# Optimization experiments

Hardware: AMD Instinct MI355X
Metric: run time of the kernel (lower is better)

## Reference

```python
import jax, jax.numpy as jnp
import numpy as np

BLOCK_SPLIT = (4, 4, 4)
GRID = 256
N_BLOCK = 64
BX = GRID // 4  # 64, per-block grid resolution along each axis
N_PTS = 4_194_304


def setup_inputs() -> dict:
    key = jax.random.key(0)
    k1, k2 = jax.random.split(key)
    aabb = jnp.array([[-1.5, -1.5, -1.5], [1.5, 1.5, 1.5]], dtype=jnp.float32)
    # points roughly inside the aabb
    xyz_sampled = jax.random.uniform(k1, (N_PTS, 3), dtype=jnp.float32) * 3.0 - 1.5
    alpha_volume = jax.random.uniform(k2, (GRID, GRID, GRID), dtype=jnp.float32)
    # per-block domains (as kilonerf global_to_local expects): block AABBs
    idx = np.stack(np.meshgrid(np.arange(4), np.arange(4), np.arange(4), indexing='ij'), -1).reshape(-1, 3)
    voxel = np.array([3.0 / 4.0] * 3)
    dmin = (-1.5 + idx * voxel).astype(np.float32)
    dmax = (dmin + voxel).astype(np.float32)
    return {"xyz_sampled": xyz_sampled, "aabb": aabb, "alpha_volume": alpha_volume,
            "domain_min": jnp.asarray(dmin), "domain_max": jnp.asarray(dmax)}


def _sample_alpha(xyz, aabb, alpha_volume, dmin, dmax):
    bs = jnp.asarray(BLOCK_SPLIT, jnp.float32)
    voxel = (aabb[1] - aabb[0]) / bs                      # per-block world size
    idx3 = jnp.floor((xyz - aabb[0]) / voxel).astype(jnp.int32)
    idx3 = jnp.clip(idx3, 0, jnp.array(BLOCK_SPLIT, jnp.int32) - 1)  # edge clamp (matches loop)
    strides = jnp.array([BLOCK_SPLIT[2] * BLOCK_SPLIT[1], BLOCK_SPLIT[2], 1], jnp.int32)
    bid = (idx3 * strides).sum(-1)                        # [N] block id in [0, 64)

    order = jnp.argsort(bid)                              # jax sort is stable; matches bucket-by-block order
    bid_s = bid[order]
    pts = xyz[order]

    # global_to_local (kilonerf): map into per-block [-1,1]^3
    local = 2.0 * (pts - dmin[bid_s]) / (dmax[bid_s] - dmin[bid_s]) - 1.0  # [N,3] (gx,gy,gz)

    # torch .view(64,1,64,64,64) is a raw contiguous reinterpretation -> plain reshape
    vols = alpha_volume.reshape(N_BLOCK, BX, BX, BX)      # [B, D, H, W]
    D = H = W = BX
    # grid_sample convention: grid x -> W axis, y -> H axis, z -> D axis; align_corners=True
    fx = (local[:, 0] + 1.0) * 0.5 * (W - 1)
    fy = (local[:, 1] + 1.0) * 0.5 * (H - 1)
    fz = (local[:, 2] + 1.0) * 0.5 * (D - 1)
    x0 = jnp.floor(fx); y0 = jnp.floor(fy); z0 = jnp.floor(fz)
    wx = fx - x0; wy = fy - y0; wz = fz - z0
    x0i = x0.astype(jnp.int32); y0i = y0.astype(jnp.int32); z0i = z0.astype(jnp.int32)

    def fetch(zi, yi, xi):
        # zeros padding for out-of-range corners (grid_sample padding_mode='zeros')
        inb = (zi >= 0) & (zi < D) & (yi >= 0) & (yi < H) & (xi >= 0) & (xi < W)
        v = vols[bid_s, jnp.clip(zi, 0, D - 1), jnp.clip(yi, 0, H - 1), jnp.clip(xi, 0, W - 1)]
        return jnp.where(inb, v, 0.0)

    out = jnp.zeros_like(fx)
    for dz, wz_ in ((0, 1.0 - wz), (1, wz)):
        for dy, wy_ in ((0, 1.0 - wy), (1, wy)):
            for dx, wx_ in ((0, 1.0 - wx), (1, wx)):
                out = out + wz_ * wy_ * wx_ * fetch(z0i + dz, y0i + dy, x0i + dx)
    return out  # [N] alpha values in block-sorted order


def reference(xyz_sampled, aabb, alpha_volume, domain_min, domain_max):
    return _sample_alpha(xyz_sampled, aabb, alpha_volume, domain_min, domain_max)
```

## Files before the change

kernel.cpp:

```cpp
#include <hip/hip_runtime.h>

#define NB     64
#define NF     4096
#define TILE   16384
#define HBLK   1024
#define DBLK   1024
#define FBLK   512
#define GBLK   256
#define SBLK   256
#define FB_TILE 4096
#define STAGE_HALF 8192

#define GLOBAL_AS __attribute__((address_space(1)))
#define LDS_AS    __attribute__((address_space(3)))

__device__ __forceinline__ int compute_bid(float px, float py, float pz,
                                           float a0x, float a0y, float a0z,
                                           float vx, float vy, float vz) {
    int ix = (int)floorf((px - a0x) / vx);
    int iy = (int)floorf((py - a0y) / vy);
    int iz = (int)floorf((pz - a0z) / vz);
    ix = min(max(ix, 0), 3);
    iy = min(max(iy, 0), 3);
    iz = min(max(iz, 0), 3);
    return ix * 16 + iy * 4 + iz;
}

__device__ __forceinline__ void quant_point(float px, float py, float pz,
        float a0x, float a0y, float a0z, float vx, float vy, float vz,
        const float* s_dn, const float* s_sc,
        int& b, int& qx, int& qy, int& qz, int& key) {
    b = compute_bid(px, py, pz, a0x, a0y, a0z, vx, vy, vz);
    float fx = (px - s_dn[3 * b])     * s_sc[3 * b];
    float fy = (py - s_dn[3 * b + 1]) * s_sc[3 * b + 1];
    float fz = (pz - s_dn[3 * b + 2]) * s_sc[3 * b + 2];
    qx = min(max(__float2int_rn(fx * 256.0f), 0), 16128);
    qy = min(max(__float2int_rn(fy * 256.0f), 0), 16128);
    qz = min(max(__float2int_rn(fz * 256.0f), 0), 16128);
    key = (b << 6) | ((qz >> 12) << 4) | ((qy >> 12) << 2) | (qx >> 12);
}

__global__ void __launch_bounds__(HBLK) hist_kernel(
        const float* __restrict__ xyz, const float* __restrict__ aabb,
        const float* __restrict__ dmin, const float* __restrict__ dmax,
        int* __restrict__ hist64, int* __restrict__ tot4096, int N, int T) {
    __shared__ int   sh[NF];
    __shared__ float s_dn[192], s_sc[192];
    const int tid = threadIdx.x, g = blockIdx.x;
    for (int l = tid; l < NF; l += HBLK) sh[l] = 0;
    if (tid < 192) { s_dn[tid] = dmin[tid]; s_sc[tid] = 63.0f / (dmax[tid] - dmin[tid]); }
    const float a0x = aabb[0], a0y = aabb[1], a0z = aabb[2];
    const float vx = (aabb[3] - a0x) * 0.25f;
    const float vy = (aabb[4] - a0y) * 0.25f;
    const float vz = (aabb[5] - a0z) * 0.25f;
    __syncthreads();
    for (int c = 0; c < TILE / (HBLK * 4); ++c) {
        int p0 = g * TILE + c * (HBLK * 4) + tid * 4;
        int b, qx, qy, qz, k;
        if (p0 + 3 < N) {
            const float4* v4 = (const float4*)(xyz + (size_t)p0 * 3);
            float4 f0 = v4[0], f1 = v4[1], f2 = v4[2];
            quant_point(f0.x, f0.y, f0.z, a0x, a0y, a0z, vx, vy, vz, s_dn, s_sc, b, qx, qy, qz, k);
            atomicAdd(&sh[k], 1);
            quant_point(f0.w, f1.x, f1.y, a0x, a0y, a0z, vx, vy, vz, s_dn, s_sc, b, qx, qy, qz, k);
            atomicAdd(&sh[k], 1);
            quant_point(f1.z, f1.w, f2.x, a0x, a0y, a0z, vx, vy, vz, s_dn, s_sc, b, qx, qy, qz, k);
            atomicAdd(&sh[k], 1);
            quant_point(f2.y, f2.z, f2.w, a0x, a0y, a0z, vx, vy, vz, s_dn, s_sc, b, qx, qy, qz, k);
            atomicAdd(&sh[k], 1);
        } else {
            for (int t = 0; t < 4; ++t) {
                int i = p0 + t;
                if (i < N) {
                    quant_point(xyz[3 * i], xyz[3 * i + 1], xyz[3 * i + 2],
                                a0x, a0y, a0z, vx, vy, vz, s_dn, s_sc, b, qx, qy, qz, k);
                    atomicAdd(&sh[k], 1);
                }
            }
        }
    }
    __syncthreads();
    for (int l = tid; l < NF; l += HBLK) {
        int c = sh[l];
        if (c) atomicAdd(&tot4096[l], c);
    }
    if (tid < NB) {
        int s = 0;
        #pragma unroll
        for (int j = 0; j < 64; ++j) s += sh[tid * 64 + j];
        hist64[tid * T + g] = s;
    }
}

__global__ void scans_kernel(int* __restrict__ hist64, int* __restrict__ tot64,
                             const int* __restrict__ tot4096,
                             int* __restrict__ foff, int* __restrict__ fcnt, int G) {
    __shared__ int sh[SBLK];
    const int t = threadIdx.x;
    if (blockIdx.x < NB) {
        const int b = blockIdx.x;
        const int L = (G + SBLK - 1) / SBLK;
        const int lo = t * L;
        const int n = min(L, max(0, G - lo));
        const int base = b * G + lo;
        int s = 0;
        for (int k = 0; k < n; ++k) s += hist64[base + k];
        sh[t] = s;
        __syncthreads();
        for (int off = 1; off < SBLK; off <<= 1) {
            int v = (t >= off) ? sh[t - off] : 0;
            __syncthreads();
            sh[t] += v;
            __syncthreads();
        }
        int excl = (t == 0) ? 0 : sh[t - 1];
        for (int k = 0; k < n; ++k) {
            int v = hist64[base + k];
            hist64[base + k] = excl;
            excl += v;
        }
        if (t == SBLK - 1) tot64[b] = sh[SBLK - 1];
    } else {
        const int L = NF / SBLK;
        int loc[16];
        int s = 0;
        #pragma unroll
        for (int j = 0; j < L; ++j) { loc[j] = tot4096[t * L + j]; s += loc[j]; }
        sh[t] = s;
        __syncthreads();
        for (int o = 1; o < SBLK; o <<= 1) {
            int v = (t >= o) ? sh[t - o] : 0;
            __syncthreads();
            sh[t] += v;
            __syncthreads();
        }
        int run = (t == 0) ? 0 : sh[t - 1];
        #pragma unroll
        for (int j = 0; j < L; ++j) {
            foff[t * L + j] = run;
            fcnt[t * L + j] = run;
            run += loc[j];
        }
        if (t == SBLK - 1) foff[NF] = run;
    }
}

__global__ void __launch_bounds__(DBLK) scatterC_kernel(
        const float* __restrict__ xyz, const float* __restrict__ aabb,
        const float* __restrict__ dmin, const float* __restrict__ dmax,
        const int* __restrict__ hist64, const int* __restrict__ tot64,
        unsigned long long* __restrict__ payloadC, int N, int T) {
    __shared__ unsigned long long stage[STAGE_HALF];
    __shared__ int   s_wh[16][NB];
    __shared__ int   s_cnt0[NB];
    __shared__ int   s_off[NB];
    __shared__ int   s_start[NB];
    __shared__ int   s_gb[NB];
    __shared__ float s_dn[192], s_sc[192];
    const int tid = threadIdx.x, g = blockIdx.x;
    const int lane = tid & 63, wv = tid >> 6;
    if (tid < NB) s_off[tid] = tot64[tid];
    if (tid < 192) { s_dn[tid] = dmin[tid]; s_sc[tid] = 63.0f / (dmax[tid] - dmin[tid]); }
    ((int*)s_wh)[tid] = 0;
    const float a0x = aabb[0], a0y = aabb[1], a0z = aabb[2];
    const float vx = (aabb[3] - a0x) * 0.25f;
    const float vy = (aabb[4] - a0y) * 0.25f;
    const float vz = (aabb[5] - a0z) * 0.25f;
    __syncthreads();
    for (int o = 1; o < NB; o <<= 1) {
        int v = (tid < NB && tid >= o) ? s_off[tid - o] : 0;
        __syncthreads();
        if (tid < NB) s_off[tid] += v;
        __syncthreads();
    }
    if (tid < NB) s_cnt0[tid] = hist64[tid * T + g] + (tid ? s_off[tid - 1] : 0);

    const unsigned long long lt = (1ull << lane) - 1ull;
    const int base_i = g * TILE + wv * 1024;
    unsigned long long cache[16];
    #pragma unroll
    for (int r = 0; r < 16; ++r) {
        int i = base_i + r * 64 + lane;
        bool valid = (i < N);
        int b = 0, qx = 0, qy = 0, qz = 0, key;
        if (valid) {
            quant_point(xyz[3 * i], xyz[3 * i + 1], xyz[3 * i + 2],
                        a0x, a0y, a0z, vx, vy, vz, s_dn, s_sc, b, qx, qy, qz, key);
        }
        unsigned long long m = __ballot(valid);
        #pragma unroll
        for (int q = 0; q < 6; ++q) {
            unsigned long long bal = __ballot((b >> q) & 1);
            m &= ((b >> q) & 1) ? bal : ~bal;
        }
        int rank = __popcll(m & lt);
        int run = valid ? s_wh[wv][b] : 0;
        if (valid && rank == 0) s_wh[wv][b] = run + __popcll(m);
        int localpos = run + rank;
        cache[r] = (unsigned long long)(unsigned)qx
                 | ((unsigned long long)(unsigned)qy << 14)
                 | ((unsigned long long)(unsigned)qz << 28)
                 | ((unsigned long long)(unsigned)b  << 42)
                 | ((unsigned long long)(unsigned)localpos << 48);
    }
    __syncthreads();
    for (int o = 1; o < 16; o <<= 1) {
        int v = (wv >= o) ? s_wh[wv - o][lane] : 0;
        __syncthreads();
        s_wh[wv][lane] += v;
        __syncthreads();
    }
    if (wv == 0) {
        int v = s_wh[15][lane];
        int incl = v;
        #pragma unroll
        for (int o = 1; o < 64; o <<= 1) {
            int u = __shfl_up(incl, o);
            if (lane >= o) incl += u;
        }
        int excl = incl - v;
        s_start[lane] = excl;
        s_gb[lane] = s_cnt0[lane] - excl;
    }
    __syncthreads();
    const int n = min(TILE, N - g * TILE);
    #pragma unroll
    for (int r = 0; r < 16; ++r) {
        int i = base_i + r * 64 + lane;
        if (i < N) {
            unsigned long long cc = cache[r];
            int b = (int)((cc >> 42) & 63);
            int localpos = (int)((cc >> 48) & 1023);
            int lidx = s_start[b] + (wv ? s_wh[wv - 1][b] : 0) + localpos;
            unsigned long long p48 = cc & ((1ull << 48) - 1);
            if (lidx < STAGE_HALF) stage[lidx] = p48;
            cache[r] = p48 | ((unsigned long long)(unsigned)lidx << 48);
        }
    }
    __syncthreads();
    {
        int nA = min(n, STAGE_HALF);
        for (int j = tid; j < nA; j += DBLK) {
            unsigned long long p = stage[j];
            int b = (int)((p >> 42) & 63);
            payloadC[s_gb[b] + j] = p;
        }
    }
    __syncthreads();
    #pragma unroll
    for (int r = 0; r < 16; ++r) {
        int i = base_i + r * 64 + lane;
        if (i < N) {
            unsigned long long cc = cache[r];
            int lidx = (int)(cc >> 48);
            if (lidx >= STAGE_HALF)
                stage[lidx - STAGE_HALF] = cc & ((1ull << 48) - 1);
        }
    }
    __syncthreads();
    for (int j = STAGE_HALF + tid; j < n; j += DBLK) {
        unsigned long long p = stage[j - STAGE_HALF];
        int b = (int)((p >> 42) & 63);
        payloadC[s_gb[b] + j] = p;
    }
}

__global__ void __launch_bounds__(FBLK) scatterF_kernel(
        const unsigned long long* __restrict__ payloadC,
        int* __restrict__ fcnt,
        unsigned long long* __restrict__ payloadF, int N) {
    __shared__ int s_fb[NF];
    const int tid = threadIdx.x, t2 = blockIdx.x;
    for (int l = tid; l < NF; l += FBLK) s_fb[l] = 0;
    __syncthreads();
    const int lo = t2 * TILE;
    const int n = min(TILE, N - lo);
    for (int j0 = tid * 4; j0 < n; j0 += FBLK * 4) {
        unsigned long long p[4];
        int m;
        if (j0 + 3 < n) {
            m = 4;
            ulonglong2 a = *(const ulonglong2*)(payloadC + lo + j0);
            ulonglong2 b2 = *(const ulonglong2*)(payloadC + lo + j0 + 2);
            p[0] = a.x; p[1] = a.y; p[2] = b2.x; p[3] = b2.y;
        } else {
            m = n - j0;
            for (int t = 0; t < m; ++t) p[t] = payloadC[lo + j0 + t];
        }
        for (int t = 0; t < m; ++t) {
            unsigned long long pp = p[t];
            int qx = (int)(pp & 16383), qy = (int)((pp >> 14) & 16383);
            int qz = (int)((pp >> 28) & 16383), b = (int)((pp >> 42) & 63);
            int key = (b << 6) | ((qz >> 12) << 4) | ((qy >> 12) << 2) | (qx >> 12);
            atomicAdd(&s_fb[key], 1);
        }
    }
    __syncthreads();
    for (int l = tid; l < NF; l += FBLK) {
        int c = s_fb[l];
        s_fb[l] = c ? atomicAdd(&fcnt[l], c) : 0;
    }
    __syncthreads();
    for (int j0 = tid * 4; j0 < n; j0 += FBLK * 4) {
        unsigned long long p[4];
        int m;
        if (j0 + 3 < n) {
            m = 4;
            ulonglong2 a = *(const ulonglong2*)(payloadC + lo + j0);
            ulonglong2 b2 = *(const ulonglong2*)(payloadC + lo + j0 + 2);
            p[0] = a.x; p[1] = a.y; p[2] = b2.x; p[3] = b2.y;
        } else {
            m = n - j0;
            for (int t = 0; t < m; ++t) p[t] = payloadC[lo + j0 + t];
        }
        for (int t = 0; t < m; ++t) {
            unsigned long long pp = p[t];
            int qx = (int)(pp & 16383), qy = (int)((pp >> 14) & 16383);
            int qz = (int)((pp >> 28) & 16383), b = (int)((pp >> 42) & 63);
            int key = (b << 6) | ((qz >> 12) << 4) | ((qy >> 12) << 2) | (qx >> 12);
            int fpos = atomicAdd(&s_fb[key], 1);
            payloadF[fpos] = (pp & ((1ull << 42) - 1))
                           | ((unsigned long long)(unsigned)(lo + j0 + t) << 42);
        }
    }
}

__global__ void __launch_bounds__(GBLK) gather_kernel(
        const float* __restrict__ vol,
        const unsigned long long* __restrict__ payloadF,
        const int* __restrict__ foff, const float* __restrict__ zf,
        float* __restrict__ out) {
    __shared__ float sv[77 * 64];
    const int tid = threadIdx.x;
    const int lane = tid & 63, wv = tid >> 6;
    const int nb = gridDim.x, d = blockIdx.x;
    const int k = (nb % 8 == 0) ? (d % 8) * (nb / 8) + (d / 8) : d;
    const int b = k >> 6;
    const int bz = ((k >> 4) & 3) * 16, by = ((k >> 2) & 3) * 16, bx = (k & 3) * 16;
    const float* vb = vol + ((size_t)b << 18);
    for (int m = wv; m < 77; m += GBLK / 64) {
        int l = m * 64 + lane;
        int z = l / 289, r = l - z * 289, y = r / 17, x = r - y * 17;
        int gz = bz + z, gy = by + y, gx = bx + x;
        bool ok = (l < 17 * 17 * 17) && (gz < 64) && (gy < 64) && (gx < 64);
        const float* src = ok ? (vb + ((gz << 12) + (gy << 6) + gx)) : zf;
        __builtin_amdgcn_global_load_lds((const GLOBAL_AS void*)src,
                                         (LDS_AS void*)(sv + m * 64), 4, 0, 0);
    }
    __syncthreads();
    const int lo = foff[k];
    const int n = foff[k + 1] - lo;
    for (int j0 = tid * 4; j0 < n; j0 += GBLK * 4) {
        unsigned long long p[4];
        int m;
        if (j0 + 3 < n) {
            m = 4;
            ulonglong2 a = *(const ulonglong2*)(payloadF + lo + j0);
            ulonglong2 b2 = *(const ulonglong2*)(payloadF + lo + j0 + 2);
            p[0] = a.x; p[1] = a.y; p[2] = b2.x; p[3] = b2.y;
        } else {
            m = n - j0;
            for (int t = 0; t < m; ++t) p[t] = payloadF[lo + j0 + t];
        }
        #pragma unroll 4
        for (int t = 0; t < m; ++t) {
            unsigned long long pp = p[t];
            int qx = (int)(pp & 16383), qy = (int)((pp >> 14) & 16383);
            int qz = (int)((pp >> 28) & 16383);
            int pos = (int)(pp >> 42);
            float wx = (qx & 255) * (1.0f / 256.0f);
            float wy = (qy & 255) * (1.0f / 256.0f);
            float wz = (qz & 255) * (1.0f / 256.0f);
            int lx = (qx >> 8) - bx, ly = (qy >> 8) - by, lz = (qz >> 8) - bz;
            int base = lz * 289 + ly * 17 + lx;
            float v000 = sv[base],       v001 = sv[base + 1];
            float v010 = sv[base + 17],  v011 = sv[base + 18];
            float v100 = sv[base + 289], v101 = sv[base + 290];
            float v110 = sv[base + 306], v111 = sv[base + 307];
            float c00 = v000 + wx * (v001 - v000);
            float c01 = v010 + wx * (v011 - v010);
            float c10 = v100 + wx * (v101 - v100);
            float c11 = v110 + wx * (v111 - v110);
            float c0 = c00 + wy * (c01 - c00);
            float c1 = c10 + wy * (c11 - c10);
            out[pos] = c0 + wz * (c1 - c0);
        }
    }
}

__global__ void fb_hist_kernel(const float* __restrict__ xyz,
                               const float* __restrict__ aabb,
                               int* __restrict__ hist, int N, int G) {
    __shared__ int s_h[NB];
    const int tid = threadIdx.x, g = blockIdx.x;
    if (tid < NB) s_h[tid] = 0;
    __syncthreads();
    const float a0x = aabb[0], a0y = aabb[1], a0z = aabb[2];
    const float vx = (aabb[3] - a0x) * 0.25f;
    const float vy = (aabb[4] - a0y) * 0.25f;
    const float vz = (aabb[5] - a0z) * 0.25f;
    for (int c = 0; c < FB_TILE / 256; ++c) {
        int i = g * FB_TILE + c * 256 + tid;
        if (i < N)
            atomicAdd(&s_h[compute_bid(xyz[3 * i], xyz[3 * i + 1], xyz[3 * i + 2],
                                       a0x, a0y, a0z, vx, vy, vz)], 1);
    }
    __syncthreads();
    if (tid < NB) hist[tid * G + g] = s_h[tid];
}

__global__ void fb_scan_kernel(int* __restrict__ hist, int* __restrict__ tot, int G) {
    __shared__ int sh[SBLK];
    const int b = blockIdx.x, t = threadIdx.x;
    const int L = (G + SBLK - 1) / SBLK;
    const int lo = t * L;
    const int n = min(L, max(0, G - lo));
    const int base = b * G + lo;
    int s = 0;
    for (int k = 0; k < n; ++k) s += hist[base + k];
    sh[t] = s;
    __syncthreads();
    for (int off = 1; off < SBLK; off <<= 1) {
        int v = (t >= off) ? sh[t - off] : 0;
        __syncthreads();
        sh[t] += v;
        __syncthreads();
    }
    int excl = (t == 0) ? 0 : sh[t - 1];
    for (int k = 0; k < n; ++k) {
        int v = hist[base + k];
        hist[base + k] = excl;
        excl += v;
    }
    if (t == SBLK - 1) tot[b] = sh[SBLK - 1];
}

__global__ void fb_scatter_kernel(const float* __restrict__ xyz,
                                  const float* __restrict__ aabb,
                                  const float* __restrict__ dmin,
                                  const float* __restrict__ dmax,
                                  const float* __restrict__ vol,
                                  const int* __restrict__ hist,
                                  const int* __restrict__ tot64,
                                  float* __restrict__ out, int N, int G) {
    __shared__ int   s_cnt[NB], s_off[NB];
    __shared__ int   s_whist[4][NB];
    __shared__ float s_dn[192], s_sc[192];
    const int tid = threadIdx.x, g = blockIdx.x;
    if (tid < NB) s_off[tid] = tot64[tid];
    if (tid < 192) { s_dn[tid] = dmin[tid]; s_sc[tid] = 63.0f / (dmax[tid] - dmin[tid]); }
    __syncthreads();
    for (int o = 1; o < NB; o <<= 1) {
        int v = (tid < NB && tid >= o) ? s_off[tid - o] : 0;
        __syncthreads();
        if (tid < NB) s_off[tid] += v;
        __syncthreads();
    }
    if (tid < NB) s_cnt[tid] = hist[tid * G + g] + (tid ? s_off[tid - 1] : 0);
    const float a0x = aabb[0], a0y = aabb[1], a0z = aabb[2];
    const float vx = (aabb[3] - a0x) * 0.25f;
    const float vy = (aabb[4] - a0y) * 0.25f;
    const float vz = (aabb[5] - a0z) * 0.25f;
    __syncthreads();
    const int lane = tid & 63, wv = tid >> 6;
    const unsigned long long lt = (1ull << lane) - 1ull;
    for (int c = 0; c < FB_TILE / 256; ++c) {
        int i = g * FB_TILE + c * 256 + tid;
        bool valid = (i < N);
        int b = 0;
        float alpha = 0.0f;
        if (valid) {
            float px = xyz[3 * i], py = xyz[3 * i + 1], pz = xyz[3 * i + 2];
            b = compute_bid(px, py, pz, a0x, a0y, a0z, vx, vy, vz);
            float fx = (px - s_dn[3 * b])     * s_sc[3 * b];
            float fy = (py - s_dn[3 * b + 1]) * s_sc[3 * b + 1];
            float fz = (pz - s_dn[3 * b + 2]) * s_sc[3 * b + 2];
            float x0f = floorf(fx), y0f = floorf(fy), z0f = floorf(fz);
            float wx = fx - x0f, wy = fy - y0f, wz = fz - z0f;
            int x0 = (int)x0f, y0 = (int)y0f, z0 = (int)z0f;
            const float* vb = vol + ((size_t)b << 18);
            auto F = [&](int zi, int yi, int xi) -> float {
                if ((unsigned)zi >= 64u || (unsigned)yi >= 64u || (unsigned)xi >= 64u)
                    return 0.0f;
                return vb[(zi << 12) + (yi << 6) + xi];
            };
            float s = 0.0f;
            s += (1.0f - wz) * (1.0f - wy) * (1.0f - wx) * F(z0,     y0,     x0);
            s += (1.0f - wz) * (1.0f - wy) * wx          * F(z0,     y0,     x0 + 1);
            s += (1.0f - wz) * wy          * (1.0f - wx) * F(z0,     y0 + 1, x0);
            s += (1.0f - wz) * wy          * wx          * F(z0,     y0 + 1, x0 + 1);
            s += wz          * (1.0f - wy) * (1.0f - wx) * F(z0 + 1, y0,     x0);
            s += wz          * (1.0f - wy) * wx          * F(z0 + 1, y0,     x0 + 1);
            s += wz          * wy          * (1.0f - wx) * F(z0 + 1, y0 + 1, x0);
            s += wz          * wy          * wx          * F(z0 + 1, y0 + 1, x0 + 1);
            alpha = s;
        }
        ((int*)s_whist)[tid] = 0;
        __syncthreads();
        unsigned long long m = __ballot(valid);
        #pragma unroll
        for (int q = 0; q < 6; ++q) {
            unsigned long long bal = __ballot((b >> q) & 1);
            m &= ((b >> q) & 1) ? bal : ~bal;
        }
        int rank = __popcll(m & lt);
        if (valid && rank == 0) s_whist[wv][b] = __popcll(m);
        __syncthreads();
        if (valid) {
            int pos = s_cnt[b] + rank;
            for (int w2 = 0; w2 < wv; ++w2) pos += s_whist[w2][b];
            out[pos] = alpha;
        }
        __syncthreads();
        if (tid < NB)
            s_cnt[tid] += s_whist[0][tid] + s_whist[1][tid] +
                          s_whist[2][tid] + s_whist[3][tid];
        __syncthreads();
    }
}

extern "C" void kernel_launch(void* const* d_in, const int* in_sizes, int n_in,
                              void* d_out, int out_size, void* d_ws, size_t ws_size,
                              hipStream_t stream) {
    const float* xyz  = (const float*)d_in[0];
    const float* aabb = (const float*)d_in[1];
    const float* vol  = (const float*)d_in[2];
    const float* dmin = (const float*)d_in[3];
    const float* dmax = (const float*)d_in[4];
    float* out = (float*)d_out;
    const int N = in_sizes[0] / 3;
    const int T = (N + TILE - 1) / TILE;

    auto align = [](size_t x) { return (x + 255) & ~(size_t)255; };
    char* ws = (char*)d_ws;
    size_t o = 0;
    unsigned long long* payloadC = (unsigned long long*)(ws + o); o += align((size_t)N * 8);
    unsigned long long* payloadF = (unsigned long long*)(ws + o); o += align((size_t)N * 8);
    int* hist64  = (int*)(ws + o); o += align((size_t)NB * T * 4);
    int* tot64   = (int*)(ws + o); o += 256;
    size_t zbase = o;
    int* tot4096 = (int*)(ws + o); o += align((size_t)NF * 4);
    int* foff    = (int*)(ws + o); o += align((size_t)(NF + 1) * 4);
    int* fcnt    = (int*)(ws + o); o += align((size_t)NF * 4);
    float* zf    = (float*)(ws + o); o += 256;
    size_t zlen = o - zbase;
    const bool fine = (N <= (1 << 22)) && (ws_size >= o);

    if (fine) {
        hipMemsetAsync(ws + zbase, 0, zlen, stream);
        hist_kernel<<<T, HBLK, 0, stream>>>(xyz, aabb, dmin, dmax,
                                            hist64, tot4096, N, T);
        scans_kernel<<<NB + 1, SBLK, 0, stream>>>(hist64, tot64, tot4096,
                                                  foff, fcnt, T);
        scatterC_kernel<<<T, DBLK, 0, stream>>>(xyz, aabb, dmin, dmax,
                                                hist64, tot64, payloadC, N, T);
        scatterF_kernel<<<T, FBLK, 0, stream>>>(payloadC, fcnt, payloadF, N);
        gather_kernel<<<NF, GBLK, 0, stream>>>(vol, payloadF, foff, zf, out);
    } else {
        const int Gf = (N + FB_TILE - 1) / FB_TILE;
        int* h = (int*)ws;
        int* t = (int*)(ws + align((size_t)NB * Gf * 4));
        fb_hist_kernel<<<Gf, 256, 0, stream>>>(xyz, aabb, h, N, Gf);
        fb_scan_kernel<<<NB, SBLK, 0, stream>>>(h, t, Gf);
        fb_scatter_kernel<<<Gf, 256, 0, stream>>>(xyz, aabb, dmin, dmax, vol,
                                                  h, t, out, N, Gf);
    }
}
```

Measured before the change: 252.8 us.

## Fuse histogram, scans and coarse scatter into one cooperative grid-synced kernel

Replaces the separate hist, scans and scatterC launches with a single cooperative kernel that keeps each tile's points quantized in registers, builds both histograms, uses grid.sync to run the prefix scans in the first 65 blocks, and then scatters. This removes one full read of xyz, one recomputation of the quantization and two kernel launches. scatterF now uses 1024 threads and keeps its payload in registers instead of re-reading it for the second pass. Risks include the cost of grid-wide barriers, whether all 256 blocks of 1024 threads with larger LDS can be co-resident, and higher register pressure.

```diff
diff --git a/kernel.cpp b/kernel.cpp
--- a/kernel.cpp
+++ b/kernel.cpp
@@ -1,11 +1,11 @@
 #include <hip/hip_runtime.h>
+#include <hip/hip_cooperative_groups.h>
 
 #define NB     64
 #define NF     4096
 #define TILE   16384
-#define HBLK   1024
 #define DBLK   1024
-#define FBLK   512
+#define FBLK   1024
 #define GBLK   256
 #define SBLK   256
 #define FB_TILE 4096
@@ -13,6 +13,8 @@
 
 #define GLOBAL_AS __attribute__((address_space(1)))
 #define LDS_AS    __attribute__((address_space(3)))
+
+namespace cg = cooperative_groups;
 
 __device__ __forceinline__ int compute_bid(float px, float py, float pz,
                                            float a0x, float a0y, float a0z,
@@ -40,117 +42,16 @@
     key = (b << 6) | ((qz >> 12) << 4) | ((qy >> 12) << 2) | (qx >> 12);
 }
 
-__global__ void __launch_bounds__(HBLK) hist_kernel(
+__global__ void __launch_bounds__(DBLK) coop_kernel(
         const float* __restrict__ xyz, const float* __restrict__ aabb,
         const float* __restrict__ dmin, const float* __restrict__ dmax,
-        int* __restrict__ hist64, int* __restrict__ tot4096, int N, int T) {
-    __shared__ int   sh[NF];
-    __shared__ float s_dn[192], s_sc[192];
-    const int tid = threadIdx.x, g = blockIdx.x;
-    for (int l = tid; l < NF; l += HBLK) sh[l] = 0;
-    if (tid < 192) { s_dn[tid] = dmin[tid]; s_sc[tid] = 63.0f / (dmax[tid] - dmin[tid]); }
-    const float a0x = aabb[0], a0y = aabb[1], a0z = aabb[2];
-    const float vx = (aabb[3] - a0x) * 0.25f;
-    const float vy = (aabb[4] - a0y) * 0.25f;
-    const float vz = (aabb[5] - a0z) * 0.25f;
-    __syncthreads();
-    for (int c = 0; c < TILE / (HBLK * 4); ++c) {
-        int p0 = g * TILE + c * (HBLK * 4) + tid * 4;
-        int b, qx, qy, qz, k;
-        if (p0 + 3 < N) {
-            const float4* v4 = (const float4*)(xyz + (size_t)p0 * 3);
-            float4 f0 = v4[0], f1 = v4[1], f2 = v4[2];
-            quant_point(f0.x, f0.y, f0.z, a0x, a0y, a0z, vx, vy, vz, s_dn, s_sc, b, qx, qy, qz, k);
-            atomicAdd(&sh[k], 1);
-            quant_point(f0.w, f1.x, f1.y, a0x, a0y, a0z, vx, vy, vz, s_dn, s_sc, b, qx, qy, qz, k);
-            atomicAdd(&sh[k], 1);
-            quant_point(f1.z, f1.w, f2.x, a0x, a0y, a0z, vx, vy, vz, s_dn, s_sc, b, qx, qy, qz, k);
-            atomicAdd(&sh[k], 1);
-            quant_point(f2.y, f2.z, f2.w, a0x, a0y, a0z, vx, vy, vz, s_dn, s_sc, b, qx, qy, qz, k);
-            atomicAdd(&sh[k], 1);
-        } else {
-            for (int t = 0; t < 4; ++t) {
-                int i = p0 + t;
-                if (i < N) {
-                    quant_point(xyz[3 * i], xyz[3 * i + 1], xyz[3 * i + 2],
-                                a0x, a0y, a0z, vx, vy, vz, s_dn, s_sc, b, qx, qy, qz, k);
-                    atomicAdd(&sh[k], 1);
-                }
-            }
-        }
-    }
-    __syncthreads();
-    for (int l = tid; l < NF; l += HBLK) {
-        int c = sh[l];
-        if (c) atomicAdd(&tot4096[l], c);
-    }
-    if (tid < NB) {
-        int s = 0;
-        #pragma unroll
-        for (int j = 0; j < 64; ++j) s += sh[tid * 64 + j];
-        hist64[tid * T + g] = s;
-    }
-}
-
-__global__ void scans_kernel(int* __restrict__ hist64, int* __restrict__ tot64,
-                             const int* __restrict__ tot4096,
-                             int* __restrict__ foff, int* __restrict__ fcnt, int G) {
-    __shared__ int sh[SBLK];
-    const int t = threadIdx.x;
-    if (blockIdx.x < NB) {
-        const int b = blockIdx.x;
-        const int L = (G + SBLK - 1) / SBLK;
-        const int lo = t * L;
-        const int n = min(L, max(0, G - lo));
-        const int base = b * G + lo;
-        int s = 0;
-        for (int k = 0; k < n; ++k) s += hist64[base + k];
-        sh[t] = s;
-        __syncthreads();
-        for (int off = 1; off < SBLK; off <<= 1) {
-            int v = (t >= off) ? sh[t - off] : 0;
-            __syncthreads();
-            sh[t] += v;
-            __syncthreads();
-        }
-        int excl = (t == 0) ? 0 : sh[t - 1];
-        for (int k = 0; k < n; ++k) {
-            int v = hist64[base + k];
-            hist64[base + k] = excl;
-            excl += v;
-        }
-        if (t == SBLK - 1) tot64[b] = sh[SBLK - 1];
-    } else {
-        const int L = NF / SBLK;
-        int loc[16];
-        int s = 0;
-        #pragma unroll
-        for (int j = 0; j < L; ++j) { loc[j] = tot4096[t * L + j]; s += loc[j]; }
-        sh[t] = s;
-        __syncthreads();
-        for (int o = 1; o < SBLK; o <<= 1) {
-            int v = (t >= o) ? sh[t - o] : 0;
-            __syncthreads();
-            sh[t] += v;
-            __syncthreads();
-        }
-        int run = (t == 0) ? 0 : sh[t - 1];
-        #pragma unroll
-        for (int j = 0; j < L; ++j) {
-            foff[t * L + j] = run;
-            fcnt[t * L + j] = run;
-            run += loc[j];
-        }
-        if (t == SBLK - 1) foff[NF] = run;
-    }
-}
-
-__global__ void __launch_bounds__(DBLK) scatterC_kernel(
-        const float* __restrict__ xyz, const float* __restrict__ aabb,
-        const float* __restrict__ dmin, const float* __restrict__ dmax,
-        const int* __restrict__ hist64, const int* __restrict__ tot64,
+        int* __restrict__ hist64, int* __restrict__ tot64,
+        int* __restrict__ tot4096, int* __restrict__ foff,
+        int* __restrict__ fcnt,
         unsigned long long* __restrict__ payloadC, int N, int T) {
+    cg::grid_group grid = cg::this_grid();
     __shared__ unsigned long long stage[STAGE_HALF];
+    __shared__ int   s_fb[NF];
     __shared__ int   s_wh[16][NB];
     __shared__ int   s_cnt0[NB];
     __shared__ int   s_off[NB];
@@ -159,21 +60,14 @@
     __shared__ float s_dn[192], s_sc[192];
     const int tid = threadIdx.x, g = blockIdx.x;
     const int lane = tid & 63, wv = tid >> 6;
-    if (tid < NB) s_off[tid] = tot64[tid];
     if (tid < 192) { s_dn[tid] = dmin[tid]; s_sc[tid] = 63.0f / (dmax[tid] - dmin[tid]); }
     ((int*)s_wh)[tid] = 0;
+    for (int l = tid; l < NF; l += DBLK) s_fb[l] = 0;
     const float a0x = aabb[0], a0y = aabb[1], a0z = aabb[2];
     const float vx = (aabb[3] - a0x) * 0.25f;
     const float vy = (aabb[4] - a0y) * 0.25f;
     const float vz = (aabb[5] - a0z) * 0.25f;
     __syncthreads();
-    for (int o = 1; o < NB; o <<= 1) {
-        int v = (tid < NB && tid >= o) ? s_off[tid - o] : 0;
-        __syncthreads();
-        if (tid < NB) s_off[tid] += v;
-        __syncthreads();
-    }
-    if (tid < NB) s_cnt0[tid] = hist64[tid * T + g] + (tid ? s_off[tid - 1] : 0);
 
     const unsigned long long lt = (1ull << lane) - 1ull;
     const int base_i = g * TILE + wv * 1024;
@@ -182,10 +76,11 @@
     for (int r = 0; r < 16; ++r) {
         int i = base_i + r * 64 + lane;
         bool valid = (i < N);
-        int b = 0, qx = 0, qy = 0, qz = 0, key;
+        int b = 0, qx = 0, qy = 0, qz = 0, key = 0;
         if (valid) {
             quant_point(xyz[3 * i], xyz[3 * i + 1], xyz[3 * i + 2],
                         a0x, a0y, a0z, vx, vy, vz, s_dn, s_sc, b, qx, qy, qz, key);
+            atomicAdd(&s_fb[key], 1);
         }
         unsigned long long m = __ballot(valid);
         #pragma unroll
@@ -210,6 +105,11 @@
         s_wh[wv][lane] += v;
         __syncthreads();
     }
+    if (tid < NB) hist64[tid * T + g] = s_wh[15][tid];
+    for (int l = tid; l < NF; l += DBLK) {
+        int c = s_fb[l];
+        if (c) atomicAdd(&tot4096[l], c);
+    }
     if (wv == 0) {
         int v = s_wh[15][lane];
         int incl = v;
@@ -218,9 +118,58 @@
             int u = __shfl_up(incl, o);
             if (lane >= o) incl += u;
         }
-        int excl = incl - v;
-        s_start[lane] = excl;
-        s_gb[lane] = s_cnt0[lane] - excl;
+        s_start[lane] = incl - v;
+    }
+    grid.sync();
+    if (g < NB) {
+        int v = (tid < T) ? hist64[g * T + tid] : 0;
+        s_fb[tid] = v;
+        __syncthreads();
+        for (int off = 1; off < DBLK; off <<= 1) {
+            int u = (tid >= off) ? s_fb[tid - off] : 0;
+            __syncthreads();
+            s_fb[tid] += u;
+            __syncthreads();
+        }
+        if (tid < T) hist64[g * T + tid] = s_fb[tid] - v;
+        if (tid == DBLK - 1) tot64[g] = s_fb[DBLK - 1];
+    } else if (g == NB) {
+        int loc[NF / DBLK];
+        int s = 0;
+        #pragma unroll
+        for (int j = 0; j < NF / DBLK; ++j) {
+            loc[j] = tot4096[tid * (NF / DBLK) + j];
+            s += loc[j];
+        }
+        s_fb[tid] = s;
+        __syncthreads();
+        for (int off = 1; off < DBLK; off <<= 1) {
+            int u = (tid >= off) ? s_fb[tid - off] : 0;
+            __syncthreads();
+            s_fb[tid] += u;
+            __syncthreads();
+        }
+        int run = (tid == 0) ? 0 : s_fb[tid - 1];
+        #pragma unroll
+        for (int j = 0; j < NF / DBLK; ++j) {
+            foff[tid * (NF / DBLK) + j] = run;
+            fcnt[tid * (NF / DBLK) + j] = run;
+            run += loc[j];
+        }
+        if (tid == DBLK - 1) foff[NF] = s_fb[DBLK - 1];
+    }
+    grid.sync();
+    if (tid < NB) s_off[tid] = tot64[tid];
+    __syncthreads();
+    for (int o = 1; o < NB; o <<= 1) {
+        int v = (tid < NB && tid >= o) ? s_off[tid - o] : 0;
+        __syncthreads();
+        if (tid < NB) s_off[tid] += v;
+        __syncthreads();
+    }
+    if (tid < NB) {
+        s_cnt0[tid] = hist64[tid * T + g] + (tid ? s_off[tid - 1] : 0);
+        s_gb[tid] = s_cnt0[tid] - s_start[tid];
     }
     __syncthreads();
     const int n = min(TILE, N - g * TILE);
@@ -275,52 +224,54 @@
     __syncthreads();
     const int lo = t2 * TILE;
     const int n = min(TILE, N - lo);
-    for (int j0 = tid * 4; j0 < n; j0 += FBLK * 4) {
-        unsigned long long p[4];
-        int m;
+    unsigned long long c[16];
+    #pragma unroll
+    for (int q = 0; q < 4; ++q) {
+        int j0 = q * (FBLK * 4) + tid * 4;
         if (j0 + 3 < n) {
-            m = 4;
             ulonglong2 a = *(const ulonglong2*)(payloadC + lo + j0);
             ulonglong2 b2 = *(const ulonglong2*)(payloadC + lo + j0 + 2);
-            p[0] = a.x; p[1] = a.y; p[2] = b2.x; p[3] = b2.y;
+            c[q * 4] = a.x; c[q * 4 + 1] = a.y;
+            c[q * 4 + 2] = b2.x; c[q * 4 + 3] = b2.y;
         } else {
-            m = n - j0;
-            for (int t = 0; t < m; ++t) p[t] = payloadC[lo + j0 + t];
-        }
-        for (int t = 0; t < m; ++t) {
-            unsigned long long pp = p[t];
-            int qx = (int)(pp & 16383), qy = (int)((pp >> 14) & 16383);
-            int qz = (int)((pp >> 28) & 16383), b = (int)((pp >> 42) & 63);
-            int key = (b << 6) | ((qz >> 12) << 4) | ((qy >> 12) << 2) | (qx >> 12);
-            atomicAdd(&s_fb[key], 1);
+            for (int t = 0; t < 4; ++t) {
+                int j = j0 + t;
+                c[q * 4 + t] = (j < n) ? payloadC[lo + j] : 0ull;
+            }
+        }
+    }
+    #pragma unroll
+    for (int q = 0; q < 4; ++q) {
+        int j0 = q * (FBLK * 4) + tid * 4;
+        for (int t = 0; t < 4; ++t) {
+            if (j0 + t < n) {
+                unsigned long long pp = c[q * 4 + t];
+                int qx = (int)(pp & 16383), qy = (int)((pp >> 14) & 16383);
+                int qz = (int)((pp >> 28) & 16383), b = (int)((pp >> 42) & 63);
+                int key = (b << 6) | ((qz >> 12) << 4) | ((qy >> 12) << 2) | (qx >> 12);
+                atomicAdd(&s_fb[key], 1);
+            }
         }
     }
     __syncthreads();
     for (int l = tid; l < NF; l += FBLK) {
-        int c = s_fb[l];
-        s_fb[l] = c ? atomicAdd(&fcnt[l], c) : 0;
-    }
-    __syncthreads();
-    for (int j0 = tid * 4; j0 < n; j0 += FBLK * 4) {
-        unsigned long long p[4];
-        int m;
-        if (j0 + 3 < n) {
-            m = 4;
-            ulonglong2 a = *(const ulonglong2*)(payloadC + lo + j0);
-            ulonglong2 b2 = *(const ulonglong2*)(payloadC + lo + j0 + 2);
-            p[0] = a.x; p[1] = a.y; p[2] = b2.x; p[3] = b2.y;
-        } else {
-            m = n - j0;
-            for (int t = 0; t < m; ++t) p[t] = payloadC[lo + j0 + t];
-        }
-        for (int t = 0; t < m; ++t) {
-            unsigned long long pp = p[t];
-            int qx = (int)(pp & 16383), qy = (int)((pp >> 14) & 16383);
-            int qz = (int)((pp >> 28) & 16383), b = (int)((pp >> 42) & 63);
-            int key = (b << 6) | ((qz >> 12) << 4) | ((qy >> 12) << 2) | (qx >> 12);
-            int fpos = atomicAdd(&s_fb[key], 1);
-            payloadF[fpos] = (pp & ((1ull << 42) - 1))
-                           | ((unsigned long long)(unsigned)(lo + j0 + t) << 42);
+        int cc = s_fb[l];
+        s_fb[l] = cc ? atomicAdd(&fcnt[l], cc) : 0;
+    }
+    __syncthreads();
+    #pragma unroll
+    for (int q = 0; q < 4; ++q) {
+        int j0 = q * (FBLK * 4) + tid * 4;
+        for (int t = 0; t < 4; ++t) {
+            if (j0 + t < n) {
+                unsigned long long pp = c[q * 4 + t];
+                int qx = (int)(pp & 16383), qy = (int)((pp >> 14) & 16383);
+                int qz = (int)((pp >> 28) & 16383), b = (int)((pp >> 42) & 63);
+                int key = (b << 6) | ((qz >> 12) << 4) | ((qy >> 12) << 2) | (qx >> 12);
+                int fpos = atomicAdd(&s_fb[key], 1);
+                payloadF[fpos] = (pp & ((1ull << 42) - 1))
+                               | ((unsigned long long)(unsigned)(lo + j0 + t) << 42);
+            }
         }
     }
 }
@@ -544,16 +495,16 @@
     int* fcnt    = (int*)(ws + o); o += align((size_t)NF * 4);
     float* zf    = (float*)(ws + o); o += 256;
     size_t zlen = o - zbase;
-    const bool fine = (N <= (1 << 22)) && (ws_size >= o);
+    const bool fine = (N <= (1 << 22)) && (ws_size >= o) && (T > NB) && (T <= 256);
 
     if (fine) {
         hipMemsetAsync(ws + zbase, 0, zlen, stream);
-        hist_kernel<<<T, HBLK, 0, stream>>>(xyz, aabb, dmin, dmax,
-                                            hist64, tot4096, N, T);
-        scans_kernel<<<NB + 1, SBLK, 0, stream>>>(hist64, tot64, tot4096,
-                                                  foff, fcnt, T);
-        scatterC_kernel<<<T, DBLK, 0, stream>>>(xyz, aabb, dmin, dmax,
-                                                hist64, tot64, payloadC, N, T);
+        void* args[] = { (void*)&xyz, (void*)&aabb, (void*)&dmin, (void*)&dmax,
+                         (void*)&hist64, (void*)&tot64, (void*)&tot4096,
+                         (void*)&foff, (void*)&fcnt, (void*)&payloadC,
+                         (void*)&N, (void*)&T };
+        hipLaunchCooperativeKernel((void*)coop_kernel, dim3(T), dim3(DBLK),
+                                   args, 0, stream);
         scatterF_kernel<<<T, FBLK, 0, stream>>>(payloadC, fcnt, payloadF, N);
         gather_kernel<<<NF, GBLK, 0, stream>>>(vol, payloadF, foff, zf, out);
     } else {
```

After: 320.9 us. 1.27x slower.
